# Kernel tuning notes

Measured on AMD Instinct MI355X. Metric: run time of the kernel, lower is better.

The kernel has to match this reference:

```python
import jax, jax.numpy as jnp
import numpy as np
import math

NEIGHBOR_RADIUS = 30.0

def _masked_softmax(logits, mask, axis):
    # mask: bool, True = keep; all-masked rows return zeros
    p = jax.nn.softmax(jnp.where(mask, logits, -1e9), axis=axis) * mask.astype(logits.dtype)
    return p / jnp.clip(jnp.sum(p, axis=axis, keepdims=True), 1e-9, None)

def _forward(agents_state, agents_mask, map_polylines, map_poly_mask,
             map_poly_type, map_tl_status, map_on_route,
             pm_w1, pm_b1, pm_w2, pm_b2, type_emb, tl_emb, route_emb,
             mo_w1, mo_b1, mo_w2, mo_b2,
             ae_w1, ae_b1, ae_w2, ae_b2, ae_w3, ae_b3,
             mr_w1, mr_b1, mr_w2, mr_b2,
             nr_w1, nr_b1, nr_w2, nr_b2,
             to_w1, to_b1, to_w2, to_b2):
    relu = jax.nn.relu
    a_mask = (agents_mask > 0.5).astype(agents_state.dtype)   # (B,N,T)
    a_feat = agents_state[..., :5]
    # ---- map polyline node encoder ----
    h = relu(map_polylines @ pm_w1 + pm_b1)                   # (B,M,L,H)
    h = relu(h @ pm_w2 + pm_b2)
    h = h.max(axis=2)                                         # (B,M,H) max-pool over points
    t_idx = jnp.clip(map_poly_type, 0, type_emb.shape[0] - 1)
    s_idx = jnp.clip(map_tl_status, 0, tl_emb.shape[0] - 1)
    r_idx = jnp.clip(map_on_route, 0, route_emb.shape[0] - 1)
    h = h + type_emb[t_idx] + tl_emb[s_idx] + route_emb[r_idx]
    h = relu(h @ mo_w1 + mo_b1) @ mo_w2 + mo_b2
    map_mask = map_poly_mask > 0.5                            # (B,M) bool
    map_node = h * map_mask[..., None].astype(h.dtype)        # (B,M,D)
    map_center = map_polylines.mean(axis=2)                   # (B,M,2)
    # ---- agent state encoder ----
    a = relu(a_feat @ ae_w1 + ae_b1)
    a = relu(a @ ae_w2 + ae_b2)
    a_emb = (a @ ae_w3 + ae_b3) * a_mask[..., None]           # (B,N,T,D)
    D = a_emb.shape[-1]
    # ---- agent -> map attention ----
    agent_pos = a_feat[..., 0:2]
    rel = map_center[:, None, None, :, :] - agent_pos[:, :, :, None, :]  # (B,N,T,M,2)
    dist = jnp.linalg.norm(rel, axis=-1, keepdims=True)
    rel_feat = jnp.concatenate([rel, dist], axis=-1)          # (B,N,T,M,3)
    rel_score = (relu(rel_feat @ mr_w1 + mr_b1) @ mr_w2 + mr_b2)[..., 0]  # (B,N,T,M)
    dot = jnp.einsum('bntd,bmd->bntm', a_emb, map_node) / math.sqrt(D)
    score_mask = jnp.broadcast_to(map_mask[:, None, None, :], dot.shape)
    attn = _masked_softmax(dot + rel_score, score_mask, axis=-1)
    map_ctx = jnp.einsum('bntm,bmd->bntd', attn, map_node)    # (B,N,T,D)
    # ---- neighbor graph attention ----
    pos = a_feat[..., 0:2]
    vel = a_feat[..., 3:5]
    pos_j = jnp.transpose(pos, (0, 2, 1, 3))                  # (B,T,N,2)
    vel_j = jnp.transpose(vel, (0, 2, 1, 3))
    rel_pos = pos_j[:, None, :, :, :] - pos[:, :, :, None, :] # (B,N,T,N,2) = p_j - p_i
    rel_vel = vel_j[:, None, :, :, :] - vel[:, :, :, None, :]
    dist_ij = jnp.linalg.norm(rel_pos, axis=-1, keepdims=True)
    rel_ij = jnp.concatenate([rel_pos, rel_vel, dist_ij], axis=-1)        # (B,N,T,N,5)
    nbr_score = (relu(rel_ij @ nr_w1 + nr_b1) @ nr_w2 + nr_b2)[..., 0]    # (B,N,T,N)
    am_b = agents_mask > 0.5
    valid_i = am_b[..., None]                                 # (B,N,T,1)
    valid_j = jnp.transpose(am_b, (0, 2, 1))[:, None, :, :]   # (B,1,T,N)
    N = pos.shape[1]
    not_self = ~jnp.eye(N, dtype=bool)[None, :, None, :]      # (1,N,1,N)
    nbr_mask = valid_i & valid_j & (dist_ij[..., 0] <= NEIGHBOR_RADIUS) & not_self
    dot_n = jnp.einsum('bitd,bjtd->bitj', a_emb, a_emb) / math.sqrt(D)
    w_n = _masked_softmax(dot_n + nbr_score, nbr_mask, axis=-1)
    nbr_ctx = jnp.einsum('bitj,bjtd->bitd', w_n, a_emb)       # (B,N,T,D)
    # ---- tau head ----
    tau = jnp.concatenate([a_emb, map_ctx, nbr_ctx], axis=-1)
    tau = relu(tau @ to_w1 + to_b1) @ to_w2 + to_b2
    return tau * a_mask[..., None]

def setup_inputs() -> dict:
    key = jax.random.key(0)
    B, N, T, M, L = 2, 32, 32, 256, 20
    H, D, TAU = 128, 128, 64
    ks = jax.random.split(key, 32)
    def f(i, shp):
        return jax.random.normal(ks[i], shp, jnp.float32) * 0.05
    inp = {}
    inp['agents_state'] = jax.random.normal(ks[0], (B, N, T, 5), jnp.float32) * jnp.array([50., 50., 1., 5., 5.], jnp.float32)
    inp['agents_mask'] = jnp.ones((B, N, T), jnp.float32)
    inp['map_polylines'] = jax.random.normal(ks[1], (B, M, L, 2), jnp.float32) * 50.0
    inp['map_poly_mask'] = jnp.ones((B, M), jnp.float32)
    inp['map_poly_type'] = jax.random.randint(ks[2], (B, M), 0, 4)
    inp['map_tl_status'] = jax.random.randint(ks[3], (B, M), 0, 8)
    inp['map_on_route'] = jax.random.randint(ks[4], (B, M), 0, 2)
    inp['pm_w1'] = f(5, (2, H));  inp['pm_b1'] = jnp.zeros((H,), jnp.float32)
    inp['pm_w2'] = f(6, (H, H)); inp['pm_b2'] = jnp.zeros((H,), jnp.float32)
    inp['type_emb'] = f(7, (4, H)); inp['tl_emb'] = f(8, (8, H)); inp['route_emb'] = f(9, (2, H))
    inp['mo_w1'] = f(10, (H, H)); inp['mo_b1'] = jnp.zeros((H,), jnp.float32)
    inp['mo_w2'] = f(11, (H, D)); inp['mo_b2'] = jnp.zeros((D,), jnp.float32)
    inp['ae_w1'] = f(12, (5, H)); inp['ae_b1'] = jnp.zeros((H,), jnp.float32)
    inp['ae_w2'] = f(13, (H, H)); inp['ae_b2'] = jnp.zeros((H,), jnp.float32)
    inp['ae_w3'] = f(14, (H, D)); inp['ae_b3'] = jnp.zeros((D,), jnp.float32)
    inp['mr_w1'] = f(15, (3, H)); inp['mr_b1'] = jnp.zeros((H,), jnp.float32)
    inp['mr_w2'] = f(16, (H, 1)); inp['mr_b2'] = jnp.zeros((1,), jnp.float32)
    inp['nr_w1'] = f(17, (5, H)); inp['nr_b1'] = jnp.zeros((H,), jnp.float32)
    inp['nr_w2'] = f(18, (H, 1)); inp['nr_b2'] = jnp.zeros((1,), jnp.float32)
    inp['to_w1'] = f(19, (3 * D, H)); inp['to_b1'] = jnp.zeros((H,), jnp.float32)
    inp['to_w2'] = f(20, (H, TAU)); inp['to_b2'] = jnp.zeros((TAU,), jnp.float32)
    return inp

def reference(agents_state, agents_mask, map_polylines, map_poly_mask,
              map_poly_type, map_tl_status, map_on_route,
              pm_w1, pm_b1, pm_w2, pm_b2, type_emb, tl_emb, route_emb,
              mo_w1, mo_b1, mo_w2, mo_b2,
              ae_w1, ae_b1, ae_w2, ae_b2, ae_w3, ae_b3,
              mr_w1, mr_b1, mr_w2, mr_b2,
              nr_w1, nr_b1, nr_w2, nr_b2,
              to_w1, to_b1, to_w2, to_b2):
    return _forward(agents_state, agents_mask, map_polylines, map_poly_mask,
                    map_poly_type, map_tl_status, map_on_route,
                    pm_w1, pm_b1, pm_w2, pm_b2, type_emb, tl_emb, route_emb,
                    mo_w1, mo_b1, mo_w2, mo_b2,
                    ae_w1, ae_b1, ae_w2, ae_b2, ae_w3, ae_b3,
                    mr_w1, mr_b1, mr_w2, mr_b2,
                    nr_w1, nr_b1, nr_w2, nr_b2,
                    to_w1, to_b1, to_w2, to_b2)
```

## Files before the change

### kernel.cpp

```cpp
#include <hip/hip_runtime.h>

#define RSQRT_D 0.08838834764831843f

__global__ __launch_bounds__(256) void kAB_front(
    const float* __restrict__ poly, const float* __restrict__ pmask,
    const int* __restrict__ ptype, const int* __restrict__ ptl, const int* __restrict__ proute,
    const float* __restrict__ pm_w1, const float* __restrict__ pm_b1,
    const float* __restrict__ pm_w2, const float* __restrict__ pm_b2,
    const float* __restrict__ type_emb, const float* __restrict__ tl_emb, const float* __restrict__ route_emb,
    const float* __restrict__ mo_w1, const float* __restrict__ mo_b1,
    const float* __restrict__ mo_w2, const float* __restrict__ mo_b2,
    const float* __restrict__ astate, const float* __restrict__ amask,
    const float* __restrict__ ae_w1, const float* __restrict__ ae_b1,
    const float* __restrict__ ae_w2, const float* __restrict__ ae_b2,
    const float* __restrict__ ae_w3, const float* __restrict__ ae_b3,
    float* __restrict__ map_node, float* __restrict__ map_nodeT, float* __restrict__ center,
    float* __restrict__ a_emb, float* __restrict__ aT, float* __restrict__ posT)
{
    int tid = threadIdx.x;
    if (blockIdx.x < 512) {
        int bm = blockIdx.x;
        int b = bm >> 8, m = bm & 255;
        int h = tid & 127, rw = tid >> 7;
        __shared__ float xch[2][128];
        __shared__ __align__(16) float hvs[128];
        __shared__ __align__(16) float g2[128];
        __shared__ __align__(16) float h1s[2][128][12];

        {
            int k = h;
            int half = rw;
            const float* pp = poly + bm*40 + half*20;
            float wx = pm_w1[k], wy = pm_w1[128+k], bb = pm_b1[k];
            float h1v[10];
            #pragma unroll
            for (int u = 0; u < 10; ++u) {
                float x = pp[2*u], y = pp[2*u+1];
                h1v[u] = fmaxf(fmaf(wx, x, fmaf(wy, y, bb)), 0.f);
            }
            float4 s0 = make_float4(h1v[0], h1v[1], h1v[2], h1v[3]);
            float4 s1 = make_float4(h1v[4], h1v[5], h1v[6], h1v[7]);
            float2 s2 = make_float2(h1v[8], h1v[9]);
            *(float4*)&h1s[half][k][0] = s0;
            *(float4*)&h1s[half][k][4] = s1;
            *(float2*)&h1s[half][k][8] = s2;
        }
        __syncthreads();

        float acc[10];
        #pragma unroll
        for (int u = 0; u < 10; ++u) acc[u] = 0.f;
        const float* w2p = pm_w2 + h;
        #pragma unroll 2
        for (int k = 0; k < 128; ++k) {
            float w2v = w2p[k*128];
            float4 A  = *(const float4*)&h1s[rw][k][0];
            float4 Bv = *(const float4*)&h1s[rw][k][4];
            float2 Cv = *(const float2*)&h1s[rw][k][8];
            acc[0] = fmaf(A.x,  w2v, acc[0]);
            acc[1] = fmaf(A.y,  w2v, acc[1]);
            acc[2] = fmaf(A.z,  w2v, acc[2]);
            acc[3] = fmaf(A.w,  w2v, acc[3]);
            acc[4] = fmaf(Bv.x, w2v, acc[4]);
            acc[5] = fmaf(Bv.y, w2v, acc[5]);
            acc[6] = fmaf(Bv.z, w2v, acc[6]);
            acc[7] = fmaf(Bv.w, w2v, acc[7]);
            acc[8] = fmaf(Cv.x, w2v, acc[8]);
            acc[9] = fmaf(Cv.y, w2v, acc[9]);
        }
        float mx = acc[0];
        #pragma unroll
        for (int u = 1; u < 10; ++u) mx = fmaxf(mx, acc[u]);
        xch[rw][h] = mx;
        __syncthreads();
        if (rw == 0) {
            float v = fmaxf(fmaxf(mx, xch[1][h]) + pm_b2[h], 0.f);
            int ti = min(max(ptype[bm],0),3);
            int si = min(max(ptl[bm],0),7);
            int ri = min(max(proute[bm],0),1);
            hvs[h] = v + type_emb[ti*128+h] + tl_emb[si*128+h] + route_emb[ri*128+h];
        }
        __syncthreads();
        {
            float a1 = (rw == 0) ? mo_b1[h] : 0.f;
            int k0 = rw * 64;
            for (int kc = 0; kc < 16; ++kc) {
                float4 xv = *(const float4*)&hvs[k0 + kc*4];
                a1 = fmaf(xv.x, mo_w1[(k0+kc*4+0)*128+h],
                     fmaf(xv.y, mo_w1[(k0+kc*4+1)*128+h],
                     fmaf(xv.z, mo_w1[(k0+kc*4+2)*128+h],
                     fmaf(xv.w, mo_w1[(k0+kc*4+3)*128+h], a1))));
            }
            xch[rw][h] = a1;
        }
        __syncthreads();
        if (tid < 128) g2[tid] = fmaxf(xch[0][tid] + xch[1][tid], 0.f);
        __syncthreads();
        {
            float a2 = (rw == 0) ? mo_b2[h] : 0.f;
            int k0 = rw * 64;
            for (int kc = 0; kc < 16; ++kc) {
                float4 xv = *(const float4*)&g2[k0 + kc*4];
                a2 = fmaf(xv.x, mo_w2[(k0+kc*4+0)*128+h],
                     fmaf(xv.y, mo_w2[(k0+kc*4+1)*128+h],
                     fmaf(xv.z, mo_w2[(k0+kc*4+2)*128+h],
                     fmaf(xv.w, mo_w2[(k0+kc*4+3)*128+h], a2))));
            }
            xch[rw][h] = a2;
        }
        __syncthreads();
        if (tid < 128) {
            float a2 = xch[0][tid] + xch[1][tid];
            float mk = (pmask[bm] > 0.5f) ? 1.f : 0.f;
            a2 *= mk;
            map_node[bm*128 + tid] = a2;
            map_nodeT[(b*128+tid)*256 + m] = a2;
        }
        if (tid == 0) {
            float sx = 0.f, sy = 0.f;
            #pragma unroll
            for (int l = 0; l < 20; ++l) { sx += poly[bm*40 + 2*l]; sy += poly[bm*40 + 2*l + 1]; }
            center[bm*2+0] = sx * 0.05f;
            center[bm*2+1] = sy * 0.05f;
        }
    } else {
        int h = tid & 127, rp = tid >> 7;
        int r0 = (blockIdx.x - 512)*8 + rp*4;
        __shared__ float f5[2][4][5];
        __shared__ __align__(16) float a1s[2][4][128];
        if (h < 20) f5[rp][h/5][h%5] = astate[(r0 + h/5)*5 + (h%5)];
        __syncthreads();
        float b1v = ae_b1[h];
        float v[4];
        {
            float w0 = ae_w1[h], w1 = ae_w1[128+h], w2 = ae_w1[256+h], w3 = ae_w1[384+h], w4 = ae_w1[512+h];
            #pragma unroll
            for (int r = 0; r < 4; ++r) {
                float a = b1v;
                a = fmaf(f5[rp][r][0], w0, a); a = fmaf(f5[rp][r][1], w1, a);
                a = fmaf(f5[rp][r][2], w2, a); a = fmaf(f5[rp][r][3], w3, a);
                a = fmaf(f5[rp][r][4], w4, a);
                v[r] = fmaxf(a, 0.f);
            }
        }
        #pragma unroll
        for (int r = 0; r < 4; ++r) a1s[rp][r][h] = v[r];
        __syncthreads();
        {
            float b2v = ae_b2[h];
            float a0 = b2v, a1 = b2v, a2 = b2v, a3 = b2v;
            for (int kc = 0; kc < 32; ++kc) {
                float4 x0 = *(const float4*)&a1s[rp][0][kc*4];
                float4 x1 = *(const float4*)&a1s[rp][1][kc*4];
                float4 x2 = *(const float4*)&a1s[rp][2][kc*4];
                float4 x3 = *(const float4*)&a1s[rp][3][kc*4];
                float w0 = ae_w2[(kc*4+0)*128+h], w1 = ae_w2[(kc*4+1)*128+h];
                float w2 = ae_w2[(kc*4+2)*128+h], w3 = ae_w2[(kc*4+3)*128+h];
                a0 = fmaf(x0.x,w0,fmaf(x0.y,w1,fmaf(x0.z,w2,fmaf(x0.w,w3,a0))));
                a1 = fmaf(x1.x,w0,fmaf(x1.y,w1,fmaf(x1.z,w2,fmaf(x1.w,w3,a1))));
                a2 = fmaf(x2.x,w0,fmaf(x2.y,w1,fmaf(x2.z,w2,fmaf(x2.w,w3,a2))));
                a3 = fmaf(x3.x,w0,fmaf(x3.y,w1,fmaf(x3.z,w2,fmaf(x3.w,w3,a3))));
            }
            v[0]=fmaxf(a0,0.f); v[1]=fmaxf(a1,0.f); v[2]=fmaxf(a2,0.f); v[3]=fmaxf(a3,0.f);
        }
        __syncthreads();
        #pragma unroll
        for (int r = 0; r < 4; ++r) a1s[rp][r][h] = v[r];
        __syncthreads();
        {
            float b3v = ae_b3[h];
            float a0 = b3v, a1 = b3v, a2 = b3v, a3 = b3v;
            for (int kc = 0; kc < 32; ++kc) {
                float4 x0 = *(const float4*)&a1s[rp][0][kc*4];
                float4 x1 = *(const float4*)&a1s[rp][1][kc*4];
                float4 x2 = *(const float4*)&a1s[rp][2][kc*4];
                float4 x3 = *(const float4*)&a1s[rp][3][kc*4];
                float w0 = ae_w3[(kc*4+0)*128+h], w1 = ae_w3[(kc*4+1)*128+h];
                float w2 = ae_w3[(kc*4+2)*128+h], w3 = ae_w3[(kc*4+3)*128+h];
                a0 = fmaf(x0.x,w0,fmaf(x0.y,w1,fmaf(x0.z,w2,fmaf(x0.w,w3,a0))));
                a1 = fmaf(x1.x,w0,fmaf(x1.y,w1,fmaf(x1.z,w2,fmaf(x1.w,w3,a1))));
                a2 = fmaf(x2.x,w0,fmaf(x2.y,w1,fmaf(x2.z,w2,fmaf(x2.w,w3,a2))));
                a3 = fmaf(x3.x,w0,fmaf(x3.y,w1,fmaf(x3.z,w2,fmaf(x3.w,w3,a3))));
            }
            v[0]=a0; v[1]=a1; v[2]=a2; v[3]=a3;
        }
        #pragma unroll
        for (int r = 0; r < 4; ++r) {
            int rr = r0 + r;
            float mk = (amask[rr] > 0.5f) ? 1.f : 0.f;
            float e = v[r] * mk;
            a_emb[rr*128 + h] = e;
            int bb = rr >> 10, nn = (rr >> 5) & 31, tt = rr & 31;
            int bt = bb*32 + tt;
            aT[(bt*128 + h)*32 + nn] = e;
        }
        if (h < 20) {
            int r = h / 5, c = h % 5;
            int rr = r0 + r;
            int bb = rr >> 10, nn = (rr >> 5) & 31, tt = rr & 31;
            int bt = bb*32 + tt;
            float val;
            if      (c == 0) val = f5[rp][r][0];
            else if (c == 1) val = f5[rp][r][1];
            else if (c == 2) val = f5[rp][r][3];
            else if (c == 3) val = f5[rp][r][4];
            else             val = amask[rr];
            posT[(bt*5 + c)*32 + nn] = val;
        }
    }
}

__global__ __launch_bounds__(512, 8) void kCD_fused(
    const float* __restrict__ astate, const float* __restrict__ amask,
    const float* __restrict__ pmask,
    const float* __restrict__ a_emb, const float* __restrict__ map_node,
    const float* __restrict__ map_nodeT, const float* __restrict__ center,
    const float* __restrict__ mr_w1, const float* __restrict__ mr_b1,
    const float* __restrict__ mr_w2, const float* __restrict__ mr_b2,
    const float* __restrict__ aT, const float* __restrict__ posT,
    const float* __restrict__ nr_w1, const float* __restrict__ nr_b1,
    const float* __restrict__ nr_w2, const float* __restrict__ nr_b2,
    const float* __restrict__ to_w1, const float* __restrict__ to_b1,
    const float* __restrict__ to_w2, const float* __restrict__ to_b2,
    float* __restrict__ out)
{
    int tid = threadIdx.x;
    int r0 = blockIdx.x * 2;
    int b = r0 >> 10, t0 = r0 & 31;

    __shared__ float lg4[2][256];
    __shared__ __align__(16) float p4[256*2];
    __shared__ float sp1[2][256];
    __shared__ float dp1[2][256];
    __shared__ float ctxp[2][128];
    __shared__ float pj[2][32];
    __shared__ __align__(16) float tau[2][384];
    __shared__ float redn[2][128];
    __shared__ __align__(16) float gpart[4][2][128];
    __shared__ __align__(16) float g1s[2][128];

    float sA0, sA1, dt0, dt1;
    {
        int m = tid & 255, kh = tid >> 8;
        float b2c = mr_b2[0];
        float cx = center[(b*256+m)*2+0], cy = center[(b*256+m)*2+1];
        float px0 = astate[(r0+0)*5+0], py0 = astate[(r0+0)*5+1];
        float px1 = astate[(r0+1)*5+0], py1 = astate[(r0+1)*5+1];
        float rx0 = cx - px0, ry0 = cy - py0;
        float rx1 = cx - px1, ry1 = cy - py1;
        float dd0 = sqrtf(rx0*rx0 + ry0*ry0);
        float dd1 = sqrtf(rx1*rx1 + ry1*ry1);
        sA0 = kh ? 0.f : b2c; sA1 = sA0;
        dt0 = 0.f; dt1 = 0.f;
        const float* mT = map_nodeT + b*128*256 + m;
        const float* ae0 = a_emb + (size_t)(r0+0)*128;
        const float* ae1 = a_emb + (size_t)(r0+1)*128;
        int h0 = kh*64;
        #pragma unroll 4
        for (int q = 0; q < 64; ++q) {
            int hh = h0 + q;
            float wa = mr_w1[hh], wb = mr_w1[128+hh], wc = mr_w1[256+hh];
            float bb = mr_b1[hh], w2 = mr_w2[hh];
            float v = mT[hh*256];
            float t10 = fmaf(rx0, wa, fmaf(ry0, wb, fmaf(dd0, wc, bb)));
            float t11 = fmaf(rx1, wa, fmaf(ry1, wb, fmaf(dd1, wc, bb)));
            sA0 = fmaf(fmaxf(t10, 0.f), w2, sA0);
            sA1 = fmaf(fmaxf(t11, 0.f), w2, sA1);
            dt0 = fmaf(v, ae0[hh], dt0);
            dt1 = fmaf(v, ae1[hh], dt1);
        }
        if (kh) { sp1[0][m] = sA0; sp1[1][m] = sA1; dp1[0][m] = dt0; dp1[1][m] = dt1; }
    }
    __syncthreads();

    if (tid < 256) {
        int m = tid;
        bool mk = pmask[b*256+m] > 0.5f;
        lg4[0][m] = mk ? fmaf(dt0 + dp1[0][m], RSQRT_D, sA0 + sp1[0][m]) : -1e30f;
        lg4[1][m] = mk ? fmaf(dt1 + dp1[1][m], RSQRT_D, sA1 + sp1[1][m]) : -1e30f;
    } else if (tid < 384) {
        int lam = tid & 63, wv = (tid >> 6) & 1;
        int r = r0 + wv;
        int ii = (r >> 5) & 31, tt = r & 31;
        int bt = b*32 + tt;
        int j = lam & 31, hs = lam >> 5;
        float pxi = astate[r*5+0], pyi = astate[r*5+1], vxi = astate[r*5+3], vyi = astate[r*5+4];
        const float* pT = posT + bt*160;
        float pxj = pT[j], pyj = pT[32+j], vxj = pT[64+j], vyj = pT[96+j], mj = pT[128+j];
        float rpx = pxj-pxi, rpy = pyj-pyi, rvx = vxj-vxi, rvy = vyj-vyi;
        float ddv = sqrtf(rpx*rpx + rpy*rpy);
        const float* ei = a_emb + (size_t)r*128;
        const float* aTp = aT + (size_t)bt*4096 + j;
        float s = 0.f, dot = 0.f;
        int h0 = hs*64;
        #pragma unroll 8
        for (int q = 0; q < 64; ++q) {
            int hh = h0 + q;
            float wA = nr_w1[hh], wB = nr_w1[128+hh], wC = nr_w1[256+hh];
            float wD = nr_w1[384+hh], wE = nr_w1[512+hh];
            float bb = nr_b1[hh], w2 = nr_w2[hh];
            float t1 = fmaf(rpx, wA, fmaf(rpy, wB, fmaf(rvx, wC,
                       fmaf(rvy, wD, fmaf(ddv, wE, bb)))));
            s = fmaf(fmaxf(t1, 0.f), w2, s);
            dot = fmaf(ei[hh], aTp[hh*32], dot);
        }
        s   += __shfl_xor(s, 32);
        dot += __shfl_xor(dot, 32);
        bool vi = amask[r] > 0.5f, vj = mj > 0.5f;
        bool ok = vi && vj && (ddv <= 30.0f) && (j != ii);
        float lg = ok ? fmaf(dot, RSQRT_D, s + nr_b2[0]) : -1e30f;
        float mxv = lg;
        #pragma unroll
        for (int off = 16; off; off >>= 1) mxv = fmaxf(mxv, __shfl_xor(mxv, off));
        float e = (lg > -1e29f) ? expf(lg - mxv) : 0.f;
        float sm = e;
        #pragma unroll
        for (int off = 16; off; off >>= 1) sm += __shfl_xor(sm, off);
        if (hs == 0) pj[wv][j] = e / fmaxf(sm, 1e-9f);
    } else {
        int d = tid & 127;
        tau[0][d] = a_emb[(size_t)r0*128 + d];
        tau[1][d] = a_emb[(size_t)(r0+1)*128 + d];
    }
    __syncthreads();

    if (tid < 128) {
        int lam = tid & 63, wv = tid >> 6;
        float x0 = lg4[wv][lam], x1 = lg4[wv][64+lam], x2 = lg4[wv][128+lam], x3 = lg4[wv][192+lam];
        float mxv = fmaxf(fmaxf(x0,x1), fmaxf(x2,x3));
        #pragma unroll
        for (int off = 32; off; off >>= 1) mxv = fmaxf(mxv, __shfl_xor(mxv, off));
        float e0 = (x0 > -1e29f) ? expf(x0-mxv) : 0.f;
        float e1 = (x1 > -1e29f) ? expf(x1-mxv) : 0.f;
        float e2 = (x2 > -1e29f) ? expf(x2-mxv) : 0.f;
        float e3 = (x3 > -1e29f) ? expf(x3-mxv) : 0.f;
        float sm = e0+e1+e2+e3;
        #pragma unroll
        for (int off = 32; off; off >>= 1) sm += __shfl_xor(sm, off);
        float inv = 1.f / fmaxf(sm, 1e-9f);
        p4[lam*2 + wv]       = e0*inv;
        p4[(64+lam)*2 + wv]  = e1*inv;
        p4[(128+lam)*2 + wv] = e2*inv;
        p4[(192+lam)*2 + wv] = e3*inv;
    }
    __syncthreads();

    float pv0 = 0.f, pv1 = 0.f;
    float na0 = 0.f, na1 = 0.f;
    if (tid < 256) {
        int d = tid & 127, hf = tid >> 7;
        const float* mn = map_node + (b*256 + hf*128)*128 + d;
        const float2* ppv = (const float2*)p4 + hf*128;
        #pragma unroll 8
        for (int mm = 0; mm < 128; ++mm) {
            float2 pvv = ppv[mm];
            float v = mn[mm*128];
            pv0 = fmaf(pvv.x, v, pv0); pv1 = fmaf(pvv.y, v, pv1);
        }
        if (hf == 1) { ctxp[0][d]=pv0; ctxp[1][d]=pv1; }
    } else {
        int local = tid - 256;
        int d = local & 127, hf = local >> 7;
        for (int jj = 0; jj < 16; ++jj) {
            int j2 = hf*16 + jj;
            float p0 = pj[0][j2], p1 = pj[1][j2];
            const float* ejb = a_emb + (size_t)((b*32 + j2)*32 + t0)*128 + d;
            na0 = fmaf(p0, ejb[0],   na0);
            na1 = fmaf(p1, ejb[128], na1);
        }
        if (hf == 1) { redn[0][d]=na0; redn[1][d]=na1; }
    }
    __syncthreads();

    if (tid < 128) {
        int d = tid;
        tau[0][128+d] = pv0 + ctxp[0][d];
        tau[1][128+d] = pv1 + ctxp[1][d];
    } else if (tid >= 256 && tid < 384) {
        int d = tid - 256;
        tau[0][256+d] = na0 + redn[0][d];
        tau[1][256+d] = na1 + redn[1][d];
    }
    __syncthreads();

    {
        int h6 = tid & 63, kq = (tid >> 6) & 3, side = tid >> 8;
        int col = side*64 + h6;
        float a0v = 0.f, a1v = 0.f;
        for (int c = 0; c < 24; ++c) {
            int k4 = kq*24 + c;
            float4 x0 = *(const float4*)&tau[0][k4*4];
            float4 x1 = *(const float4*)&tau[1][k4*4];
            float w0 = to_w1[(k4*4+0)*128 + col];
            float w1 = to_w1[(k4*4+1)*128 + col];
            float w2 = to_w1[(k4*4+2)*128 + col];
            float w3 = to_w1[(k4*4+3)*128 + col];
            a0v = fmaf(x0.x,w0,fmaf(x0.y,w1,fmaf(x0.z,w2,fmaf(x0.w,w3,a0v))));
            a1v = fmaf(x1.x,w0,fmaf(x1.y,w1,fmaf(x1.z,w2,fmaf(x1.w,w3,a1v))));
        }
        gpart[kq][0][col] = a0v;
        gpart[kq][1][col] = a1v;
    }
    __syncthreads();

    if (tid < 256) {
        int h = tid & 127, rr = tid >> 7;
        float s = gpart[0][rr][h] + gpart[1][rr][h] + gpart[2][rr][h] + gpart[3][rr][h];
        g1s[rr][h] = fmaxf(s + to_b1[h], 0.f);
    }
    __syncthreads();

    if (tid < 128) {
        int o = tid & 63, row = tid >> 6;
        float a2 = to_b2[o];
        for (int kc = 0; kc < 32; ++kc) {
            float4 g = *(const float4*)&g1s[row][kc*4];
            a2 = fmaf(g.x, to_w2[(kc*4+0)*64 + o],
                 fmaf(g.y, to_w2[(kc*4+1)*64 + o],
                 fmaf(g.z, to_w2[(kc*4+2)*64 + o],
                 fmaf(g.w, to_w2[(kc*4+3)*64 + o], a2))));
        }
        float mk = (amask[r0+row] > 0.5f) ? 1.f : 0.f;
        out[(r0+row)*64 + o] = a2 * mk;
    }
}

extern "C" void kernel_launch(void* const* d_in, const int* in_sizes, int n_in,
                              void* d_out, int out_size, void* d_ws, size_t ws_size,
                              hipStream_t stream) {
    const float* agents_state  = (const float*)d_in[0];
    const float* agents_mask   = (const float*)d_in[1];
    const float* map_polylines = (const float*)d_in[2];
    const float* map_poly_mask = (const float*)d_in[3];
    const int*   map_poly_type = (const int*)d_in[4];
    const int*   map_tl_status = (const int*)d_in[5];
    const int*   map_on_route  = (const int*)d_in[6];
    const float* pm_w1 = (const float*)d_in[7];
    const float* pm_b1 = (const float*)d_in[8];
    const float* pm_w2 = (const float*)d_in[9];
    const float* pm_b2 = (const float*)d_in[10];
    const float* type_emb  = (const float*)d_in[11];
    const float* tl_emb    = (const float*)d_in[12];
    const float* route_emb = (const float*)d_in[13];
    const float* mo_w1 = (const float*)d_in[14];
    const float* mo_b1 = (const float*)d_in[15];
    const float* mo_w2 = (const float*)d_in[16];
    const float* mo_b2 = (const float*)d_in[17];
    const float* ae_w1 = (const float*)d_in[18];
    const float* ae_b1 = (const float*)d_in[19];
    const float* ae_w2 = (const float*)d_in[20];
    const float* ae_b2 = (const float*)d_in[21];
    const float* ae_w3 = (const float*)d_in[22];
    const float* ae_b3 = (const float*)d_in[23];
    const float* mr_w1 = (const float*)d_in[24];
    const float* mr_b1 = (const float*)d_in[25];
    const float* mr_w2 = (const float*)d_in[26];
    const float* mr_b2 = (const float*)d_in[27];
    const float* nr_w1 = (const float*)d_in[28];
    const float* nr_b1 = (const float*)d_in[29];
    const float* nr_w2 = (const float*)d_in[30];
    const float* nr_b2 = (const float*)d_in[31];
    const float* to_w1 = (const float*)d_in[32];
    const float* to_b1 = (const float*)d_in[33];
    const float* to_w2 = (const float*)d_in[34];
    const float* to_b2 = (const float*)d_in[35];

    float* ws = (float*)d_ws;
    float* map_node  = ws;
    float* map_nodeT = ws + 65536;
    float* center    = ws + 131072;
    float* a_emb     = ws + 132096;
    float* aT        = ws + 394240;
    float* posT      = ws + 656384;

    float* out = (float*)d_out;

    kAB_front<<<768, 256, 0, stream>>>(map_polylines, map_poly_mask,
        map_poly_type, map_tl_status, map_on_route,
        pm_w1, pm_b1, pm_w2, pm_b2, type_emb, tl_emb, route_emb,
        mo_w1, mo_b1, mo_w2, mo_b2,
        agents_state, agents_mask,
        ae_w1, ae_b1, ae_w2, ae_b2, ae_w3, ae_b3,
        map_node, map_nodeT, center, a_emb, aT, posT);

    kCD_fused<<<1024, 512, 0, stream>>>(agents_state, agents_mask, map_poly_mask,
        a_emb, map_node, map_nodeT, center,
        mr_w1, mr_b1, mr_w2, mr_b2,
        aT, posT,
        nr_w1, nr_b1, nr_w2, nr_b2,
        to_w1, to_b1, to_w2, to_b2,
        out);
}
```

Baseline: 211.0 us.

## Process eight agent rows per block in fused attention kernel for weight reuse

The fused attention/output kernel now handles eight (agent,time) rows per 1024-thread block instead of two per 512-thread block. Each map-node, weight and embedding load is amortised over eight rows in registers, and the map-score, neighbor-attention and output MLP phases are reorganised to match. This cuts redundant global/L2 traffic for map_nodeT, map_node and to_w1. In exchange the grid shrinks to 256 blocks, per-thread register pressure rises, and shared memory per block grows, which could reduce occupancy on the GPU.

```diff
diff --git a/kernel.cpp b/kernel.cpp
--- a/kernel.cpp
+++ b/kernel.cpp
@@ -210,7 +210,7 @@
     }
 }
 
-__global__ __launch_bounds__(512, 8) void kCD_fused(
+__global__ __launch_bounds__(1024, 4) void kCD_fused(
     const float* __restrict__ astate, const float* __restrict__ amask,
     const float* __restrict__ pmask,
     const float* __restrict__ a_emb, const float* __restrict__ map_node,
@@ -225,36 +225,36 @@
     float* __restrict__ out)
 {
     int tid = threadIdx.x;
-    int r0 = blockIdx.x * 2;
+    int r0 = blockIdx.x * 8;
     int b = r0 >> 10, t0 = r0 & 31;
 
-    __shared__ float lg4[2][256];
-    __shared__ __align__(16) float p4[256*2];
-    __shared__ float sp1[2][256];
-    __shared__ float dp1[2][256];
-    __shared__ float ctxp[2][128];
-    __shared__ float pj[2][32];
-    __shared__ __align__(16) float tau[2][384];
-    __shared__ float redn[2][128];
-    __shared__ __align__(16) float gpart[4][2][128];
-    __shared__ __align__(16) float g1s[2][128];
-
-    float sA0, sA1, dt0, dt1;
-    {
+    __shared__ float sp[8][256];
+    __shared__ float dp[8][256];
+    __shared__ float lg4[8][256];
+    __shared__ __align__(16) float p4[256*8];
+    __shared__ float pj[8][32];
+    __shared__ __align__(16) float tau[8][384];
+    __shared__ float pvp[4][8][128];
+    __shared__ float nrp[4][8][128];
+    __shared__ __align__(16) float gpart[4][8][128];
+    __shared__ __align__(16) float g1s[8][128];
+
+    float sA[8], dt[8];
+    if (tid < 512) {
         int m = tid & 255, kh = tid >> 8;
         float b2c = mr_b2[0];
         float cx = center[(b*256+m)*2+0], cy = center[(b*256+m)*2+1];
-        float px0 = astate[(r0+0)*5+0], py0 = astate[(r0+0)*5+1];
-        float px1 = astate[(r0+1)*5+0], py1 = astate[(r0+1)*5+1];
-        float rx0 = cx - px0, ry0 = cy - py0;
-        float rx1 = cx - px1, ry1 = cy - py1;
-        float dd0 = sqrtf(rx0*rx0 + ry0*ry0);
-        float dd1 = sqrtf(rx1*rx1 + ry1*ry1);
-        sA0 = kh ? 0.f : b2c; sA1 = sA0;
-        dt0 = 0.f; dt1 = 0.f;
+        float rx[8], ry[8], dd[8];
+        #pragma unroll
+        for (int r = 0; r < 8; ++r) {
+            float px = astate[(r0+r)*5+0], py = astate[(r0+r)*5+1];
+            rx[r] = cx - px; ry[r] = cy - py;
+            dd[r] = sqrtf(rx[r]*rx[r] + ry[r]*ry[r]);
+            sA[r] = kh ? 0.f : b2c;
+            dt[r] = 0.f;
+        }
         const float* mT = map_nodeT + b*128*256 + m;
-        const float* ae0 = a_emb + (size_t)(r0+0)*128;
-        const float* ae1 = a_emb + (size_t)(r0+1)*128;
+        const float* ae = a_emb + (size_t)r0*128;
         int h0 = kh*64;
         #pragma unroll 4
         for (int q = 0; q < 64; ++q) {
@@ -262,24 +262,20 @@
             float wa = mr_w1[hh], wb = mr_w1[128+hh], wc = mr_w1[256+hh];
             float bb = mr_b1[hh], w2 = mr_w2[hh];
             float v = mT[hh*256];
-            float t10 = fmaf(rx0, wa, fmaf(ry0, wb, fmaf(dd0, wc, bb)));
-            float t11 = fmaf(rx1, wa, fmaf(ry1, wb, fmaf(dd1, wc, bb)));
-            sA0 = fmaf(fmaxf(t10, 0.f), w2, sA0);
-            sA1 = fmaf(fmaxf(t11, 0.f), w2, sA1);
-            dt0 = fmaf(v, ae0[hh], dt0);
-            dt1 = fmaf(v, ae1[hh], dt1);
-        }
-        if (kh) { sp1[0][m] = sA0; sp1[1][m] = sA1; dp1[0][m] = dt0; dp1[1][m] = dt1; }
-    }
-    __syncthreads();
-
-    if (tid < 256) {
-        int m = tid;
-        bool mk = pmask[b*256+m] > 0.5f;
-        lg4[0][m] = mk ? fmaf(dt0 + dp1[0][m], RSQRT_D, sA0 + sp1[0][m]) : -1e30f;
-        lg4[1][m] = mk ? fmaf(dt1 + dp1[1][m], RSQRT_D, sA1 + sp1[1][m]) : -1e30f;
-    } else if (tid < 384) {
-        int lam = tid & 63, wv = (tid >> 6) & 1;
+            #pragma unroll
+            for (int r = 0; r < 8; ++r) {
+                float t1 = fmaf(rx[r], wa, fmaf(ry[r], wb, fmaf(dd[r], wc, bb)));
+                sA[r] = fmaf(fmaxf(t1, 0.f), w2, sA[r]);
+                dt[r] = fmaf(v, ae[r*128 + hh], dt[r]);
+            }
+        }
+        if (kh) {
+            #pragma unroll
+            for (int r = 0; r < 8; ++r) { sp[r][m] = sA[r]; dp[r][m] = dt[r]; }
+        }
+    } else {
+        int local = tid - 512;
+        int lam = local & 63, wv = local >> 6;
         int r = r0 + wv;
         int ii = (r >> 5) & 31, tt = r & 31;
         int bt = b*32 + tt;
@@ -317,14 +313,27 @@
         #pragma unroll
         for (int off = 16; off; off >>= 1) sm += __shfl_xor(sm, off);
         if (hs == 0) pj[wv][j] = e / fmaxf(sm, 1e-9f);
-    } else {
-        int d = tid & 127;
-        tau[0][d] = a_emb[(size_t)r0*128 + d];
-        tau[1][d] = a_emb[(size_t)(r0+1)*128 + d];
-    }
-    __syncthreads();
-
-    if (tid < 128) {
+    }
+    __syncthreads();
+
+    if (tid < 256) {
+        int m = tid;
+        bool mk = pmask[b*256+m] > 0.5f;
+        #pragma unroll
+        for (int r = 0; r < 8; ++r)
+            lg4[r][m] = mk ? fmaf(dt[r] + dp[r][m], RSQRT_D, sA[r] + sp[r][m]) : -1e30f;
+    } else if (tid < 512) {
+        int idx = tid - 256;
+        int d = idx & 127, rq = idx >> 7;
+        #pragma unroll
+        for (int k = 0; k < 4; ++k) {
+            int rr = rq*4 + k;
+            tau[rr][d] = a_emb[(size_t)(r0+rr)*128 + d];
+        }
+    }
+    __syncthreads();
+
+    if (tid < 512) {
         int lam = tid & 63, wv = tid >> 6;
         float x0 = lg4[wv][lam], x1 = lg4[wv][64+lam], x2 = lg4[wv][128+lam], x3 = lg4[wv][192+lam];
         float mxv = fmaxf(fmaxf(x0,x1), fmaxf(x2,x3));
@@ -338,79 +347,91 @@
         #pragma unroll
         for (int off = 32; off; off >>= 1) sm += __shfl_xor(sm, off);
         float inv = 1.f / fmaxf(sm, 1e-9f);
-        p4[lam*2 + wv]       = e0*inv;
-        p4[(64+lam)*2 + wv]  = e1*inv;
-        p4[(128+lam)*2 + wv] = e2*inv;
-        p4[(192+lam)*2 + wv] = e3*inv;
-    }
-    __syncthreads();
-
-    float pv0 = 0.f, pv1 = 0.f;
-    float na0 = 0.f, na1 = 0.f;
-    if (tid < 256) {
-        int d = tid & 127, hf = tid >> 7;
-        const float* mn = map_node + (b*256 + hf*128)*128 + d;
-        const float2* ppv = (const float2*)p4 + hf*128;
-        #pragma unroll 8
-        for (int mm = 0; mm < 128; ++mm) {
-            float2 pvv = ppv[mm];
+        p4[lam*8 + wv]       = e0*inv;
+        p4[(64+lam)*8 + wv]  = e1*inv;
+        p4[(128+lam)*8 + wv] = e2*inv;
+        p4[(192+lam)*8 + wv] = e3*inv;
+    }
+    __syncthreads();
+
+    if (tid < 512) {
+        int d = tid & 127, mq = tid >> 7;
+        const float* mn = map_node + (b*256 + mq*64)*128 + d;
+        const float* pq = p4 + (mq*64)*8;
+        float pv[8];
+        #pragma unroll
+        for (int r = 0; r < 8; ++r) pv[r] = 0.f;
+        #pragma unroll 4
+        for (int mm = 0; mm < 64; ++mm) {
             float v = mn[mm*128];
-            pv0 = fmaf(pvv.x, v, pv0); pv1 = fmaf(pvv.y, v, pv1);
-        }
-        if (hf == 1) { ctxp[0][d]=pv0; ctxp[1][d]=pv1; }
+            float4 pa = *(const float4*)&pq[mm*8];
+            float4 pb = *(const float4*)&pq[mm*8 + 4];
+            pv[0] = fmaf(pa.x, v, pv[0]); pv[1] = fmaf(pa.y, v, pv[1]);
+            pv[2] = fmaf(pa.z, v, pv[2]); pv[3] = fmaf(pa.w, v, pv[3]);
+            pv[4] = fmaf(pb.x, v, pv[4]); pv[5] = fmaf(pb.y, v, pv[5]);
+            pv[6] = fmaf(pb.z, v, pv[6]); pv[7] = fmaf(pb.w, v, pv[7]);
+        }
+        #pragma unroll
+        for (int r = 0; r < 8; ++r) pvp[mq][r][d] = pv[r];
     } else {
-        int local = tid - 256;
-        int d = local & 127, hf = local >> 7;
-        for (int jj = 0; jj < 16; ++jj) {
-            int j2 = hf*16 + jj;
-            float p0 = pj[0][j2], p1 = pj[1][j2];
+        int local = tid - 512;
+        int d = local & 127, jq = local >> 7;
+        float na[8];
+        #pragma unroll
+        for (int r = 0; r < 8; ++r) na[r] = 0.f;
+        for (int jj = 0; jj < 8; ++jj) {
+            int j2 = jq*8 + jj;
             const float* ejb = a_emb + (size_t)((b*32 + j2)*32 + t0)*128 + d;
-            na0 = fmaf(p0, ejb[0],   na0);
-            na1 = fmaf(p1, ejb[128], na1);
-        }
-        if (hf == 1) { redn[0][d]=na0; redn[1][d]=na1; }
-    }
-    __syncthreads();
-
-    if (tid < 128) {
-        int d = tid;
-        tau[0][128+d] = pv0 + ctxp[0][d];
-        tau[1][128+d] = pv1 + ctxp[1][d];
-    } else if (tid >= 256 && tid < 384) {
-        int d = tid - 256;
-        tau[0][256+d] = na0 + redn[0][d];
-        tau[1][256+d] = na1 + redn[1][d];
+            #pragma unroll
+            for (int r = 0; r < 8; ++r)
+                na[r] = fmaf(pj[r][j2], ejb[r*128], na[r]);
+        }
+        #pragma unroll
+        for (int r = 0; r < 8; ++r) nrp[jq][r][d] = na[r];
     }
     __syncthreads();
 
     {
-        int h6 = tid & 63, kq = (tid >> 6) & 3, side = tid >> 8;
-        int col = side*64 + h6;
-        float a0v = 0.f, a1v = 0.f;
+        int d = tid & 127, r = tid >> 7;
+        tau[r][128+d] = pvp[0][r][d] + pvp[1][r][d] + pvp[2][r][d] + pvp[3][r][d];
+        tau[r][256+d] = nrp[0][r][d] + nrp[1][r][d] + nrp[2][r][d] + nrp[3][r][d];
+    }
+    __syncthreads();
+
+    {
+        int col = tid & 127, kq = (tid >> 7) & 3, rg = tid >> 9;
+        int rb = rg*4;
+        float a0v = 0.f, a1v = 0.f, a2v = 0.f, a3v = 0.f;
         for (int c = 0; c < 24; ++c) {
             int k4 = kq*24 + c;
-            float4 x0 = *(const float4*)&tau[0][k4*4];
-            float4 x1 = *(const float4*)&tau[1][k4*4];
+            float4 x0 = *(const float4*)&tau[rb+0][k4*4];
+            float4 x1 = *(const float4*)&tau[rb+1][k4*4];
+            float4 x2 = *(const float4*)&tau[rb+2][k4*4];
+            float4 x3 = *(const float4*)&tau[rb+3][k4*4];
             float w0 = to_w1[(k4*4+0)*128 + col];
             float w1 = to_w1[(k4*4+1)*128 + col];
             float w2 = to_w1[(k4*4+2)*128 + col];
             float w3 = to_w1[(k4*4+3)*128 + col];
             a0v = fmaf(x0.x,w0,fmaf(x0.y,w1,fmaf(x0.z,w2,fmaf(x0.w,w3,a0v))));
             a1v = fmaf(x1.x,w0,fmaf(x1.y,w1,fmaf(x1.z,w2,fmaf(x1.w,w3,a1v))));
-        }
-        gpart[kq][0][col] = a0v;
-        gpart[kq][1][col] = a1v;
-    }
-    __syncthreads();
-
-    if (tid < 256) {
+            a2v = fmaf(x2.x,w0,fmaf(x2.y,w1,fmaf(x2.z,w2,fmaf(x2.w,w3,a2v))));
+            a3v = fmaf(x3.x,w0,fmaf(x3.y,w1,fmaf(x3.z,w2,fmaf(x3.w,w3,a3v))));
+        }
+        gpart[kq][rb+0][col] = a0v;
+        gpart[kq][rb+1][col] = a1v;
+        gpart[kq][rb+2][col] = a2v;
+        gpart[kq][rb+3][col] = a3v;
+    }
+    __syncthreads();
+
+    {
         int h = tid & 127, rr = tid >> 7;
         float s = gpart[0][rr][h] + gpart[1][rr][h] + gpart[2][rr][h] + gpart[3][rr][h];
         g1s[rr][h] = fmaxf(s + to_b1[h], 0.f);
     }
     __syncthreads();
 
-    if (tid < 128) {
+    if (tid < 512) {
         int o = tid & 63, row = tid >> 6;
         float a2 = to_b2[o];
         for (int kc = 0; kc < 32; ++kc) {
@@ -483,7 +504,7 @@
         ae_w1, ae_b1, ae_w2, ae_b2, ae_w3, ae_b3,
         map_node, map_nodeT, center, a_emb, aT, posT);
 
-    kCD_fused<<<1024, 512, 0, stream>>>(agents_state, agents_mask, map_poly_mask,
+    kCD_fused<<<256, 1024, 0, stream>>>(agents_state, agents_mask, map_poly_mask,
         a_emb, map_node, map_nodeT, center,
         mr_w1, mr_b1, mr_w2, mr_b2,
         aT, posT,
```

Measured after the change: 189.0 us. 1.12x faster.
